# Performance work log

Hardware: AMD Instinct MI355X
Metric: run time of the kernel (lower is better)

The kernel has to match this reference:

```python
import jax, jax.numpy as jnp
import numpy as np
from jax import lax

EPS = 1e-5
DN = ('NCHW', 'OIHW', 'NCHW')


def _bn(x, gamma, beta, mean, var):
    # eval-mode BatchNorm2d over channel dim (axis=1)
    s = gamma / jnp.sqrt(var + EPS)
    return x * s[None, :, None, None] + (beta - mean * s)[None, :, None, None]


def setup_inputs() -> dict:
    key = jax.random.key(0)
    ks = jax.random.split(key, 12)
    B, Cin, C, H, W, NC = 128, 2048, 512, 14, 14, 200
    return {
        'feature': jax.random.normal(ks[0], (B, Cin, H, W), jnp.float32),
        'w_reduce': jax.random.normal(ks[1], (C, Cin, 1, 1), jnp.float32) * 0.02,
        'b_reduce': jax.random.normal(ks[2], (C,), jnp.float32) * 0.02,
        'bn1_gamma': jnp.ones((C,), jnp.float32),
        'bn1_beta': jnp.zeros((C,), jnp.float32),
        'bn1_mean': jax.random.normal(ks[3], (C,), jnp.float32) * 0.02,
        'bn1_var': jax.random.uniform(ks[4], (C,), jnp.float32),
        'w3': jax.random.normal(ks[5], (C, C, 3, 3), jnp.float32) * 0.02,
        'b3': jax.random.normal(ks[6], (C,), jnp.float32) * 0.02,
        'bn2_gamma': jnp.ones((C,), jnp.float32),
        'bn2_beta': jnp.zeros((C,), jnp.float32),
        'bn2_mean': jax.random.normal(ks[7], (C,), jnp.float32) * 0.02,
        'bn2_var': jax.random.uniform(ks[8], (C,), jnp.float32),
        'fc1_w': jax.random.normal(ks[9], (NC, C), jnp.float32) * 0.02,
        'fc1_b': jnp.zeros((NC,), jnp.float32),
        'fc2_w': jax.random.normal(ks[10], (NC, NC), jnp.float32) * 0.02,
        'fc2_b': jnp.zeros((NC,), jnp.float32),
    }


def reference(feature, w_reduce, b_reduce, bn1_gamma, bn1_beta, bn1_mean, bn1_var,
              w3, b3, bn2_gamma, bn2_beta, bn2_mean, bn2_var,
              fc1_w, fc1_b, fc2_w, fc2_b):
    B, _, H, W = feature.shape
    C = w_reduce.shape[0]  # 512
    # reduce: 1x1 conv + BN + ReLU
    f = lax.conv_general_dilated(feature, w_reduce, (1, 1), 'VALID', dimension_numbers=DN)
    f = f + b_reduce[None, :, None, None]
    f = jax.nn.relu(_bn(f, bn1_gamma, bn1_beta, bn1_mean, bn1_var))
    x = f.reshape(B, C, H * W)  # [B, 512, 196]
    # channel affinity + softmax(-xxt) over last dim (= the per-row loop)
    xxt = jnp.einsum('bcn,bdn->bcd', x, x)  # [B, 512, 512]
    a = jax.nn.softmax(-xxt, axis=2)
    y = jnp.einsum('bcd,bdn->bcn', a, x).reshape(B, C, H, W)
    # conv3: 3x3 conv + BN + ReLU + global avg pool
    z = lax.conv_general_dilated(y, w3, (1, 1), 'SAME', dimension_numbers=DN)
    z = z + b3[None, :, None, None]
    z = jax.nn.relu(_bn(z, bn2_gamma, bn2_beta, bn2_mean, bn2_var))
    z = jnp.mean(z, axis=(2, 3))  # [B, 512]
    # fc_channel: Linear -> ReLU -> Linear
    h = jax.nn.relu(z @ fc1_w.T + fc1_b)
    sf = h @ fc2_w.T + fc2_b
    return sf
```

## Files before the change

### kernel.cpp

```cpp
#include <hip/hip_runtime.h>

typedef __attribute__((ext_vector_type(8))) short bf16x8;
typedef __attribute__((ext_vector_type(4))) float f32x4;
typedef __attribute__((ext_vector_type(4))) short short4v;

__device__ __forceinline__ unsigned short f2bf(float x){
  unsigned u = __float_as_uint(x);
  return (unsigned short)((u + 0x7FFFu + ((u>>16)&1u)) >> 16);
}
__device__ __forceinline__ float bf2f(unsigned short b){
  return __uint_as_float(((unsigned)b)<<16);
}

typedef const __attribute__((address_space(1))) void* gas_t;
typedef __attribute__((address_space(3))) void* las_t;
__device__ __forceinline__ void gl16(const void* g, void* l){
  __builtin_amdgcn_global_load_lds((gas_t)g, (las_t)l, 16, 0, 0);
}

static constexpr size_t O_A    = 0;
static constexpr size_t O_FTLO = 29360128;
static constexpr size_t O_XHI  = 134217728;
static constexpr size_t O_XLO  = 167772160;
static constexpr size_t O_XT   = 201326592;
static constexpr size_t O_AMAT = 230686720;
static constexpr size_t O_WH   = 297795584;
static constexpr size_t O_WL   = 299892736;
static constexpr size_t O_W3B  = 301989888;
static constexpr size_t O_PAR  = 306708480;
static constexpr size_t O_FC1T = 306716672;
static constexpr size_t O_FC2T = 307126272;
static constexpr size_t O_ZBAR = 307286272;

__global__ void k_params(const float* br, const float* g1, const float* be1, const float* m1, const float* v1,
                         const float* b3, const float* g2, const float* be2, const float* m2, const float* v2,
                         float* par){
  int c = blockIdx.x*256 + threadIdx.x;
  if (c >= 512) return;
  float s1 = g1[c] * rsqrtf(v1[c] + 1e-5f);
  par[c] = s1;
  par[512+c] = (br[c]-m1[c])*s1 + be1[c];
  float s2 = g2[c] * rsqrtf(v2[c] + 1e-5f);
  par[1024+c] = s2;
  par[1536+c] = (b3[c]-m2[c])*s2 + be2[c];
}

__global__ void k_wrhl(const float* wr, unsigned short* wh, unsigned short* wl){
  int k = blockIdx.x*256 + threadIdx.x;
  int c = blockIdx.y;
  float v = wr[(size_t)c*2048 + k];
  unsigned short h = f2bf(v);
  wh[(size_t)c*2048 + k] = h;
  wl[(size_t)c*2048 + k] = f2bf(v - bf2f(h));
}

__global__ void k_w3c(const float* w3, unsigned short* w3c){
  int k = blockIdx.x*256 + threadIdx.x;
  int co = blockIdx.y;
  int ci0b = k/576; int r2 = k - ci0b*576;
  int tap = r2>>6;  int cio = r2&63;
  w3c[(((size_t)ci0b*9 + tap)*512 + co)*64 + cio] =
      f2bf(w3[((size_t)co*512 + ci0b*64 + cio)*9 + tap]);
}

__global__ void k_fc1t(const float* w, float* wt){
  int i = blockIdx.x*256 + threadIdx.x;
  int k = i/200, j = i - k*200;
  wt[i] = w[j*512 + k];
}
__global__ void k_fc2t(const float* w, float* wt){
  int i = blockIdx.x*256 + threadIdx.x;
  if (i >= 200*200) return;
  int k = i/200, j = i - k*200;
  wt[i] = w[j*200 + k];
}

__global__ __launch_bounds__(256) void k_featT(const float* __restrict__ feat,
        unsigned short* __restrict__ fhi, unsigned short* __restrict__ flo, int bbase){
  __shared__ float tile[64][33];
  int bloc = blockIdx.z;
  int b = bbase + bloc;
  int ci0 = blockIdx.y*64, p0 = blockIdx.x*32;
  int t = threadIdx.x;
  int j = t & 31, i0 = t >> 5;
  for (int rep=0; rep<8; ++rep){
    int i = rep*8 + i0;
    int p = p0 + j;
    tile[i][j] = (p<196) ? feat[((size_t)b*2048 + ci0 + i)*196 + p] : 0.f;
  }
  __syncthreads();
  int ii = t & 63, jj0 = t >> 6;
  for (int rep=0; rep<8; ++rep){
    int jj = rep*4 + jj0;
    float v = tile[ii][jj];
    unsigned short h = f2bf(v);
    size_t o = ((size_t)bloc*224 + p0 + jj)*2048 + ci0 + ii;
    fhi[o] = h;
    flo[o] = f2bf(v - bf2f(h));
  }
}

__global__ __launch_bounds__(256) void k_conv1(
    const unsigned short* __restrict__ fhi, const unsigned short* __restrict__ flo,
    const unsigned short* __restrict__ wh,  const unsigned short* __restrict__ wl,
    const float* __restrict__ par,
    unsigned short* __restrict__ xhi, unsigned short* __restrict__ xlo,
    unsigned short* __restrict__ xT, int bbase){
  __shared__ char lds[61440];
  char* AH = lds;
  char* ALo = lds + 16384;
  char* BH = lds + 32768;
  char* BLo = lds + 47104;
  int lin = blockIdx.x, per = gridDim.x>>3;
  int sz  = (lin&7)*per + (lin>>3);
  int bloc = sz>>3, sub = sz&7, mt = sub>>1, nt = sub&1;
  int b = bbase + bloc;
  int c0 = mt*128, n0 = nt*112;
  int t = threadIdx.x, lane = t&63, wid = t>>6;
  int fq = lane>>4, fr = lane&15;
  f32x4 acc[2][7] = {};
  const unsigned short* fbh = fhi + (size_t)bloc*224*2048;
  const unsigned short* fbl = flo + (size_t)bloc*224*2048;
  for (int it=0; it<32; ++it){
    int k0 = it*64;
    __syncthreads();
    #pragma unroll
    for (int r=0;r<4;++r){
      int L = r*256 + t;
      int row = L>>3, cs = ((L&7)^(row&7))*8;
      gl16(wh + (size_t)(c0+row)*2048 + k0 + cs, AH + L*16);
      gl16(wl + (size_t)(c0+row)*2048 + k0 + cs, ALo + L*16);
    }
    #pragma unroll
    for (int r=0;r<4;++r){
      int L = r*256 + t;
      if (L < 896){
        int row = L>>3, cs = ((L&7)^(row&7))*8;
        gl16(fbh + (size_t)(n0+row)*2048 + k0 + cs, BH + L*16);
        gl16(fbl + (size_t)(n0+row)*2048 + k0 + cs, BLo + L*16);
      }
    }
    __syncthreads();
    #pragma unroll
    for (int ks=0; ks<2; ++ks){
      int kb = ks*64 + fq*16;
      bf16x8 ah[2], al2[2];
      #pragma unroll
      for (int m=0;m<2;++m){
        int row = wid*32 + m*16 + fr;
        int off = row*128 + (kb ^ ((row&7)<<4));
        ah[m]  = *(const bf16x8*)(AH + off);
        al2[m] = *(const bf16x8*)(ALo + off);
      }
      #pragma unroll
      for (int n=0;n<7;++n){
        int row = n*16 + fr;
        int off = row*128 + (kb ^ ((row&7)<<4));
        bf16x8 bh  = *(const bf16x8*)(BH + off);
        bf16x8 bl2 = *(const bf16x8*)(BLo + off);
        #pragma unroll
        for (int m=0;m<2;++m){
          acc[m][n] = __builtin_amdgcn_mfma_f32_16x16x32_bf16(ah[m],  bh,  acc[m][n],0,0,0);
          acc[m][n] = __builtin_amdgcn_mfma_f32_16x16x32_bf16(ah[m],  bl2, acc[m][n],0,0,0);
          acc[m][n] = __builtin_amdgcn_mfma_f32_16x16x32_bf16(al2[m], bh,  acc[m][n],0,0,0);
        }
      }
    }
  }
  const float* s1 = par; const float* t1 = par+512;
  for (int m=0;m<2;++m){
    int cb = c0 + wid*32 + m*16 + fq*4;
    float sc[4], sh[4];
    for (int j=0;j<4;++j){ sc[j]=s1[cb+j]; sh[j]=t1[cb+j]; }
    for (int n=0;n<7;++n){
      int p = n0 + n*16 + fr;
      bool inb = p < 196;
      for (int j=0;j<4;++j){
        float v = inb ? fmaxf(acc[m][n][j]*sc[j]+sh[j], 0.f) : 0.f;
        unsigned short h  = f2bf(v);
        unsigned short lo = f2bf(v - bf2f(h));
        size_t ic = (size_t)b*512 + cb + j;
        xhi[ic*256 + p] = h;
        xlo[ic*256 + p] = lo;
        xT[((size_t)b*224 + p)*512 + cb + j] = h;
      }
    }
  }
}

__global__ __launch_bounds__(256) void k_xxt(const unsigned short* __restrict__ xhi,
        const unsigned short* __restrict__ xlo, float* __restrict__ xxt){
  __shared__ char lds[32768];
  char* Als = lds; char* Bls = lds + 16384;
  int lin = blockIdx.x;
  int sz  = (lin&7)*160 + (lin>>3);
  int b = sz/10, sub = sz - b*10;
  unsigned mtp = (3u<<18)|(2u<<16)|(2u<<14)|(1u<<12)|(1u<<10)|(1u<<8)|(0u<<6)|(0u<<4)|(0u<<2)|0u;
  unsigned ntp = (3u<<18)|(3u<<16)|(2u<<14)|(3u<<12)|(2u<<10)|(1u<<8)|(3u<<6)|(2u<<4)|(1u<<2)|0u;
  int mt = (mtp>>(2*sub))&3, nt = (ntp>>(2*sub))&3;
  int c0 = mt*128, d0 = nt*128;
  int t = threadIdx.x, lane = t&63, wid = t>>6, wm = wid&1, wn = wid>>1;
  int fq = lane>>4, fr = lane&15;
  f32x4 acc[4][4] = {};
  for (int it=0; it<12; ++it){
    int seg = it>>2, kk0 = (it&3)*64;
    const unsigned short* As = (seg<2) ? xhi : xlo;
    const unsigned short* Bs = (seg==1) ? xlo : xhi;
    __syncthreads();
    #pragma unroll
    for (int r=0;r<4;++r){
      int L = r*256 + t;
      int row = L>>3, cs = ((L&7)^(row&7))*8;
      gl16(As + ((size_t)b*512 + c0 + row)*256 + kk0 + cs, Als + L*16);
      gl16(Bs + ((size_t)b*512 + d0 + row)*256 + kk0 + cs, Bls + L*16);
    }
    __syncthreads();
    #pragma unroll
    for (int ks=0; ks<2; ++ks){
      int kb = ks*64 + fq*16;
      bf16x8 af[4];
      #pragma unroll
      for (int m=0;m<4;++m){
        int row = wm*64 + m*16 + fr;
        af[m] = *(const bf16x8*)(Als + row*128 + (kb ^ ((row&7)<<4)));
      }
      #pragma unroll
      for (int n=0;n<4;++n){
        int row = wn*64 + n*16 + fr;
        bf16x8 bff = *(const bf16x8*)(Bls + row*128 + (kb ^ ((row&7)<<4)));
        #pragma unroll
        for (int m=0;m<4;++m)
          acc[m][n] = __builtin_amdgcn_mfma_f32_16x16x32_bf16(af[m], bff, acc[m][n],0,0,0);
      }
    }
  }
  for (int m=0;m<4;++m){
    int cb = c0 + wm*64 + m*16 + fq*4;
    for (int n=0;n<4;++n){
      int d = d0 + wn*64 + n*16 + fr;
      *(float4*)(xxt + ((size_t)b*512 + d)*512 + cb) = *(float4*)&acc[m][n];
    }
  }
  if (mt != nt){
    for (int m=0;m<4;++m){
      int cb = c0 + wm*64 + m*16 + fq*4;
      for (int n=0;n<4;++n){
        int d = d0 + wn*64 + n*16 + fr;
        for (int jj=0;jj<4;++jj)
          xxt[((size_t)b*512 + cb + jj)*512 + d] = acc[m][n][jj];
      }
    }
  }
}

__global__ __launch_bounds__(256) void k_softmax(const float* __restrict__ xxt, unsigned short* __restrict__ amat){
  int row = blockIdx.x*4 + (threadIdx.x>>6);
  int lane = threadIdx.x & 63;
  const float* src = xxt + (size_t)row*512 + lane*8;
  float4 v0 = *(const float4*)src;
  float4 v1 = *(const float4*)(src+4);
  float mn = fminf(fminf(fminf(v0.x,v0.y),fminf(v0.z,v0.w)),
                   fminf(fminf(v1.x,v1.y),fminf(v1.z,v1.w)));
  for (int m=32; m; m>>=1) mn = fminf(mn, __shfl_xor(mn, m, 64));
  float e[8];
  e[0]=__expf(mn-v0.x); e[1]=__expf(mn-v0.y); e[2]=__expf(mn-v0.z); e[3]=__expf(mn-v0.w);
  e[4]=__expf(mn-v1.x); e[5]=__expf(mn-v1.y); e[6]=__expf(mn-v1.z); e[7]=__expf(mn-v1.w);
  float s = e[0]+e[1]+e[2]+e[3]+e[4]+e[5]+e[6]+e[7];
  for (int m=32; m; m>>=1) s += __shfl_xor(s, m, 64);
  float inv = 1.f/s;
  short4v p0, p1;
  for (int q=0;q<4;++q) p0[q] = (short)f2bf(e[q]*inv);
  for (int q=0;q<4;++q) p1[q] = (short)f2bf(e[4+q]*inv);
  unsigned short* dst = amat + (size_t)row*512 + lane*8;
  *(short4v*)dst = p0;
  *(short4v*)(dst+4) = p1;
}

__global__ __launch_bounds__(256) void k_pv(const unsigned short* __restrict__ amat,
        const unsigned short* __restrict__ xT, unsigned short* __restrict__ ypad){
  __shared__ char lds[30720];
  char* Als = lds; char* Bls = lds + 16384;
  int lin = blockIdx.x, per = gridDim.x>>3;
  int sz  = (lin&7)*per + (lin>>3);
  int b = sz>>3, sub = sz&7, mt = sub>>1, nt = sub&1;
  int c0 = mt*128, n0 = nt*112;
  int t = threadIdx.x, lane = t&63, wid = t>>6;
  int fq = lane>>4, fr = lane&15;
  f32x4 acc[2][7] = {};
  for (int it=0; it<8; ++it){
    int k0 = it*64;
    __syncthreads();
    #pragma unroll
    for (int r=0;r<4;++r){
      int L = r*256 + t;
      int row = L>>3, cs = ((L&7)^(row&7))*8;
      gl16(amat + ((size_t)b*512 + c0 + row)*512 + k0 + cs, Als + L*16);
    }
    #pragma unroll
    for (int r=0;r<4;++r){
      int L = r*256 + t;
      if (L < 896){
        int row = L>>3, cs = ((L&7)^(row&7))*8;
        gl16(xT + ((size_t)b*224 + n0 + row)*512 + k0 + cs, Bls + L*16);
      }
    }
    __syncthreads();
    #pragma unroll
    for (int ks=0; ks<2; ++ks){
      int kb = ks*64 + fq*16;
      bf16x8 af[2];
      #pragma unroll
      for (int m=0;m<2;++m){
        int row = wid*32 + m*16 + fr;
        af[m] = *(const bf16x8*)(Als + row*128 + (kb ^ ((row&7)<<4)));
      }
      #pragma unroll
      for (int n=0;n<7;++n){
        int row = n*16 + fr;
        bf16x8 bff = *(const bf16x8*)(Bls + row*128 + (kb ^ ((row&7)<<4)));
        #pragma unroll
        for (int m=0;m<2;++m)
          acc[m][n] = __builtin_amdgcn_mfma_f32_16x16x32_bf16(af[m], bff, acc[m][n],0,0,0);
      }
    }
  }
  for (int m=0;m<2;++m){
    int cb = c0 + wid*32 + m*16 + fq*4;
    int ci0b = cb>>6, cio = cb&63;
    for (int n=0;n<7;++n){
      int p = n0 + n*16 + fr;
      if (p < 196){
        int hh = p/14, wwp = p - hh*14;
        int prow = (hh+1)*16 + (wwp+1);
        short4v pk;
        for (int j=0;j<4;++j) pk[j] = (short)f2bf(acc[m][n][j]);
        *(short4v*)(ypad + (((size_t)b*8 + ci0b)*256 + prow)*64 + cio) = pk;
      }
    }
  }
}

__global__ __launch_bounds__(512, 4) void k_conv3(const unsigned short* __restrict__ ypad,
        const unsigned short* __restrict__ w3c, const float* __restrict__ par,
        float* __restrict__ zbar){
  __shared__ char lds[65536];
  char* WIN = lds;
  char* AB0 = lds + 32768;
  char* AB1 = lds + 49152;
  int bx = blockIdx.x;
  int xcd = bx&7, jj2 = bx>>3;
  int b = xcd*16 + (jj2>>2), cot = jj2&3;
  int c0 = cot*128;
  int t = threadIdx.x, lane = t&63, w = t>>6;
  int wm = w>>1, wn = w&1;
  int fq = lane>>4, fr = lane&15;
  int frB = (fr<14) ? fr : 13;
  bool pok = (fr<14);
  f32x4 acc[2][7] = {};
  for (int ci0=0; ci0<8; ++ci0){
    const unsigned short* wsrc = ypad + ((size_t)(b*8 + ci0)*256)*64;
    #pragma unroll
    for (int r=0;r<4;++r){
      int L = r*512 + t;
      int row = L>>3, cs = ((L&7)^(row&7))*8;
      gl16(wsrc + row*64 + cs, WIN + L*16);
    }
    {
      const unsigned short* asrc = w3c + ((size_t)(ci0*9 + 0)*512 + c0)*64;
      #pragma unroll
      for (int r=0;r<2;++r){
        int L = r*512 + t;
        int row = L>>3, cs = ((L&7)^(row&7))*8;
        gl16(asrc + row*64 + cs, AB0 + L*16);
      }
    }
    __syncthreads();
    for (int tap=0; tap<9; ++tap){
      char* Acur = (tap&1) ? AB1 : AB0;
      char* Anxt = (tap&1) ? AB0 : AB1;
      if (tap < 8){
        const unsigned short* asrc = w3c + ((size_t)(ci0*9 + tap+1)*512 + c0)*64;
        #pragma unroll
        for (int r=0;r<2;++r){
          int L = r*512 + t;
          int row = L>>3, cs = ((L&7)^(row&7))*8;
          gl16(asrc + row*64 + cs, Anxt + L*16);
        }
      }
      int kh = tap/3, kw = tap - kh*3;
      bf16x8 ah[2][2];
      #pragma unroll
      for (int ks=0;ks<2;++ks)
        #pragma unroll
        for (int m=0;m<2;++m){
          int row = wm*32 + m*16 + fr;
          ah[ks][m] = *(const bf16x8*)(Acur + row*128 + (((ks*4+fq)^(row&7))<<4));
        }
      int col = frB + kw;
      __builtin_amdgcn_s_setprio(1);
      #pragma unroll
      for (int n=0;n<7;++n){
        int prow = (wn*7 + n + kh)*16 + col;
        #pragma unroll
        for (int ks=0;ks<2;++ks){
          bf16x8 bf = *(const bf16x8*)(WIN + prow*128 + (((ks*4+fq)^(prow&7))<<4));
          acc[0][n] = __builtin_amdgcn_mfma_f32_16x16x32_bf16(ah[ks][0], bf, acc[0][n],0,0,0);
          acc[1][n] = __builtin_amdgcn_mfma_f32_16x16x32_bf16(ah[ks][1], bf, acc[1][n],0,0,0);
        }
      }
      __builtin_amdgcn_s_setprio(0);
      __syncthreads();
    }
  }
  const float* s2 = par+1024; const float* t2 = par+1536;
  float ps[2][4];
  #pragma unroll
  for (int m=0;m<2;++m){
    int cb = c0 + wm*32 + m*16 + fq*4;
    #pragma unroll
    for (int j=0;j<4;++j){
      float sc = s2[cb+j], sh = t2[cb+j];
      float s = 0.f;
      #pragma unroll
      for (int n=0;n<7;++n)
        s += fmaxf(acc[m][n][j]*sc + sh, 0.f);
      ps[m][j] = pok ? s : 0.f;
    }
  }
  #pragma unroll
  for (int off=1; off<16; off<<=1)
    #pragma unroll
    for (int m=0;m<2;++m)
      #pragma unroll
      for (int j=0;j<4;++j)
        ps[m][j] += __shfl_xor(ps[m][j], off, 64);
  float* part = (float*)lds;
  if (fr == 0){
    #pragma unroll
    for (int m=0;m<2;++m)
      #pragma unroll
      for (int j=0;j<4;++j)
        part[wn*128 + wm*32 + m*16 + fq*4 + j] = ps[m][j];
  }
  __syncthreads();
  if (t < 128)
    zbar[(size_t)b*512 + c0 + t] = part[t] + part[128 + t];
}

__global__ __launch_bounds__(256) void k_fc(const float* __restrict__ zbar,
        const float* __restrict__ fc1T, const float* __restrict__ fc1b,
        const float* __restrict__ fc2T, const float* __restrict__ fc2b,
        float* __restrict__ out){
  __shared__ float zb[512];
  __shared__ float hl[200];
  int b = blockIdx.x, t = threadIdx.x;
  zb[t]     = zbar[(size_t)b*512 + t]       * (1.f/196.f);
  zb[t+256] = zbar[(size_t)b*512 + t + 256] * (1.f/196.f);
  __syncthreads();
  if (t < 200){
    float acc = fc1b[t];
    for (int k=0;k<512;++k) acc += zb[k]*fc1T[k*200+t];
    hl[t] = fmaxf(acc, 0.f);
  }
  __syncthreads();
  if (t < 200){
    float acc = fc2b[t];
    for (int k=0;k<200;++k) acc += hl[k]*fc2T[k*200+t];
    out[(size_t)b*200 + t] = acc;
  }
}

extern "C" void kernel_launch(void* const* d_in, const int* in_sizes, int n_in,
                              void* d_out, int out_size, void* d_ws, size_t ws_size,
                              hipStream_t stream) {
  const float* feature  = (const float*)d_in[0];
  const float* w_reduce = (const float*)d_in[1];
  const float* b_reduce = (const float*)d_in[2];
  const float* g1  = (const float*)d_in[3];
  const float* be1 = (const float*)d_in[4];
  const float* m1  = (const float*)d_in[5];
  const float* v1  = (const float*)d_in[6];
  const float* w3  = (const float*)d_in[7];
  const float* b3  = (const float*)d_in[8];
  const float* g2  = (const float*)d_in[9];
  const float* be2 = (const float*)d_in[10];
  const float* m2  = (const float*)d_in[11];
  const float* v2  = (const float*)d_in[12];
  const float* fc1w = (const float*)d_in[13];
  const float* fc1b = (const float*)d_in[14];
  const float* fc2w = (const float*)d_in[15];
  const float* fc2b = (const float*)d_in[16];

  char* ws = (char*)d_ws;
  unsigned short* fhi  = (unsigned short*)(ws + O_A);
  unsigned short* flo  = (unsigned short*)(ws + O_FTLO);
  float*          xxt  = (float*)(ws + O_A);
  unsigned short* xhi  = (unsigned short*)(ws + O_XHI);
  unsigned short* xlo  = (unsigned short*)(ws + O_XLO);
  unsigned short* ypad = (unsigned short*)(ws + O_XLO);
  unsigned short* xT   = (unsigned short*)(ws + O_XT);
  unsigned short* amat = (unsigned short*)(ws + O_AMAT);
  unsigned short* wh   = (unsigned short*)(ws + O_WH);
  unsigned short* wl   = (unsigned short*)(ws + O_WL);
  unsigned short* w3c  = (unsigned short*)(ws + O_W3B);
  float* par  = (float*)(ws + O_PAR);
  float* fc1T = (float*)(ws + O_FC1T);
  float* fc2T = (float*)(ws + O_FC2T);
  float* zbar = (float*)(ws + O_ZBAR);

  hipMemsetAsync(xhi, 0, 33554432, stream);
  hipMemsetAsync(xlo, 0, 33554432, stream);

  k_params<<<2, 256, 0, stream>>>(b_reduce, g1, be1, m1, v1, b3, g2, be2, m2, v2, par);
  k_wrhl<<<dim3(8,512), 256, 0, stream>>>(w_reduce, wh, wl);
  k_w3c<<<dim3(18,512), 256, 0, stream>>>(w3, w3c);
  k_fc1t<<<400, 256, 0, stream>>>(fc1w, fc1T);
  k_fc2t<<<157, 256, 0, stream>>>(fc2w, fc2T);

  for (int ch = 0; ch < 4; ++ch){
    k_featT<<<dim3(7,32,32), 256, 0, stream>>>(feature, fhi, flo, ch*32);
    k_conv1<<<256, 256, 0, stream>>>(fhi, flo, wh, wl, par, xhi, xlo, xT, ch*32);
  }

  k_xxt<<<1280, 256, 0, stream>>>(xhi, xlo, xxt);
  k_softmax<<<16384, 256, 0, stream>>>(xxt, amat);

  hipMemsetAsync(ypad, 0, 33554432, stream);
  k_pv<<<1024, 256, 0, stream>>>(amat, xT, ypad);
  k_conv3<<<512, 512, 0, stream>>>(ypad, w3c, par, zbar);
  k_fc<<<128, 256, 0, stream>>>(zbar, fc1T, fc1b, fc2T, fc2b, (float*)d_out);
}
```

Before: 685.4 us.

## Flatten conv1 over batch-pixel GEMM with 128x128 tiles; replace full memsets with pad zeroing

The 1x1 reduce conv now runs as one GEMM over all 128*196 pixel columns without per-image padding to 224. It uses 128x128 tiles and runs the three hi/lo split products as consecutive K segments instead of three MFMAs per fragment, which removes the chunked 4-launch loop and the wasted padded columns. The full 32MB memsets are replaced by small kernels that zero only the pad regions of xhi/xlo and the border of ypad. The xT store is vectorised. The trade-offs are a larger workspace, since the whole fhi/flo for all batches is now materialised at once, and three times more K iterations per tile.

```diff
diff --git a/kernel.cpp b/kernel.cpp
--- a/kernel.cpp
+++ b/kernel.cpp
@@ -18,19 +18,19 @@
   __builtin_amdgcn_global_load_lds((gas_t)g, (las_t)l, 16, 0, 0);
 }
 
-static constexpr size_t O_A    = 0;
-static constexpr size_t O_FTLO = 29360128;
-static constexpr size_t O_XHI  = 134217728;
-static constexpr size_t O_XLO  = 167772160;
-static constexpr size_t O_XT   = 201326592;
-static constexpr size_t O_AMAT = 230686720;
-static constexpr size_t O_WH   = 297795584;
-static constexpr size_t O_WL   = 299892736;
-static constexpr size_t O_W3B  = 301989888;
-static constexpr size_t O_PAR  = 306708480;
-static constexpr size_t O_FC1T = 306716672;
-static constexpr size_t O_FC2T = 307126272;
-static constexpr size_t O_ZBAR = 307286272;
+static constexpr size_t O_FHI  = 0;
+static constexpr size_t O_FLO  = 102760448;
+static constexpr size_t O_XHI  = 205520896;
+static constexpr size_t O_XLO  = 239075328;
+static constexpr size_t O_XT   = 272629760;
+static constexpr size_t O_AMAT = 301989888;
+static constexpr size_t O_WH   = 369098752;
+static constexpr size_t O_WL   = 371195904;
+static constexpr size_t O_W3B  = 373293056;
+static constexpr size_t O_PAR  = 378011648;
+static constexpr size_t O_FC1T = 378019840;
+static constexpr size_t O_FC2T = 378429440;
+static constexpr size_t O_ZBAR = 378589440;
 
 __global__ void k_params(const float* br, const float* g1, const float* be1, const float* m1, const float* v1,
                          const float* b3, const float* g2, const float* be2, const float* m2, const float* v2,
@@ -75,11 +75,32 @@
   wt[i] = w[j*200 + k];
 }
 
+__global__ __launch_bounds__(256) void k_zeropad(unsigned short* xhi, unsigned short* xlo){
+  int rr = blockIdx.x*256 + threadIdx.x;
+  float4 z = {0.f,0.f,0.f,0.f};
+  float4* a = (float4*)(xhi + (size_t)rr*256 + 192);
+  float4* b = (float4*)(xlo + (size_t)rr*256 + 192);
+  #pragma unroll
+  for (int j=0;j<8;++j){ a[j] = z; b[j] = z; }
+}
+
+__global__ __launch_bounds__(256) void k_zeroyb(unsigned short* ypad){
+  int tile = blockIdx.x;
+  int r = threadIdx.x;
+  if (r >= 256) return;
+  int hi = r>>4, lo = r&15;
+  bool pad = (hi==0)||(hi==15)||(lo==0)||(lo==15);
+  if (!pad) return;
+  float4 z = {0.f,0.f,0.f,0.f};
+  float4* p = (float4*)(ypad + ((size_t)tile*256 + r)*64);
+  #pragma unroll
+  for (int j=0;j<8;++j) p[j] = z;
+}
+
 __global__ __launch_bounds__(256) void k_featT(const float* __restrict__ feat,
-        unsigned short* __restrict__ fhi, unsigned short* __restrict__ flo, int bbase){
+        unsigned short* __restrict__ fhi, unsigned short* __restrict__ flo){
   __shared__ float tile[64][33];
-  int bloc = blockIdx.z;
-  int b = bbase + bloc;
+  int b = blockIdx.z;
   int ci0 = blockIdx.y*64, p0 = blockIdx.x*32;
   int t = threadIdx.x;
   int j = t & 31, i0 = t >> 5;
@@ -92,11 +113,14 @@
   int ii = t & 63, jj0 = t >> 6;
   for (int rep=0; rep<8; ++rep){
     int jj = rep*4 + jj0;
-    float v = tile[ii][jj];
-    unsigned short h = f2bf(v);
-    size_t o = ((size_t)bloc*224 + p0 + jj)*2048 + ci0 + ii;
-    fhi[o] = h;
-    flo[o] = f2bf(v - bf2f(h));
+    int p = p0 + jj;
+    if (p < 196){
+      float v = tile[ii][jj];
+      unsigned short h = f2bf(v);
+      size_t o = ((size_t)b*196 + p)*2048 + ci0 + ii;
+      fhi[o] = h;
+      flo[o] = f2bf(v - bf2f(h));
+    }
   }
 }
 
@@ -105,85 +129,68 @@
     const unsigned short* __restrict__ wh,  const unsigned short* __restrict__ wl,
     const float* __restrict__ par,
     unsigned short* __restrict__ xhi, unsigned short* __restrict__ xlo,
-    unsigned short* __restrict__ xT, int bbase){
-  __shared__ char lds[61440];
-  char* AH = lds;
-  char* ALo = lds + 16384;
-  char* BH = lds + 32768;
-  char* BLo = lds + 47104;
-  int lin = blockIdx.x, per = gridDim.x>>3;
-  int sz  = (lin&7)*per + (lin>>3);
-  int bloc = sz>>3, sub = sz&7, mt = sub>>1, nt = sub&1;
-  int b = bbase + bloc;
-  int c0 = mt*128, n0 = nt*112;
-  int t = threadIdx.x, lane = t&63, wid = t>>6;
+    unsigned short* __restrict__ xT){
+  __shared__ char lds[32768];
+  char* Als = lds; char* Bls = lds + 16384;
+  int lin = blockIdx.x;
+  int sz  = (lin&7)*98 + (lin>>3);
+  int mt = sz&3;
+  int gt = sz>>2;
+  int c0 = mt*128;
+  size_t g0 = (size_t)gt*128;
+  int t = threadIdx.x, lane = t&63, wid = t>>6, wm = wid&1, wn = wid>>1;
   int fq = lane>>4, fr = lane&15;
-  f32x4 acc[2][7] = {};
-  const unsigned short* fbh = fhi + (size_t)bloc*224*2048;
-  const unsigned short* fbl = flo + (size_t)bloc*224*2048;
-  for (int it=0; it<32; ++it){
-    int k0 = it*64;
+  f32x4 acc[4][4] = {};
+  for (int it=0; it<96; ++it){
+    int seg = it>>5, kk0 = (it&31)*64;
+    const unsigned short* As = (seg<2) ? wh : wl;
+    const unsigned short* Bs = (seg==1) ? flo : fhi;
     __syncthreads();
     #pragma unroll
     for (int r=0;r<4;++r){
       int L = r*256 + t;
       int row = L>>3, cs = ((L&7)^(row&7))*8;
-      gl16(wh + (size_t)(c0+row)*2048 + k0 + cs, AH + L*16);
-      gl16(wl + (size_t)(c0+row)*2048 + k0 + cs, ALo + L*16);
-    }
-    #pragma unroll
-    for (int r=0;r<4;++r){
-      int L = r*256 + t;
-      if (L < 896){
-        int row = L>>3, cs = ((L&7)^(row&7))*8;
-        gl16(fbh + (size_t)(n0+row)*2048 + k0 + cs, BH + L*16);
-        gl16(fbl + (size_t)(n0+row)*2048 + k0 + cs, BLo + L*16);
-      }
+      gl16(As + (size_t)(c0+row)*2048 + kk0 + cs, Als + L*16);
+      gl16(Bs + (g0+row)*2048 + kk0 + cs, Bls + L*16);
     }
     __syncthreads();
     #pragma unroll
     for (int ks=0; ks<2; ++ks){
       int kb = ks*64 + fq*16;
-      bf16x8 ah[2], al2[2];
-      #pragma unroll
-      for (int m=0;m<2;++m){
-        int row = wid*32 + m*16 + fr;
-        int off = row*128 + (kb ^ ((row&7)<<4));
-        ah[m]  = *(const bf16x8*)(AH + off);
-        al2[m] = *(const bf16x8*)(ALo + off);
-      }
-      #pragma unroll
-      for (int n=0;n<7;++n){
-        int row = n*16 + fr;
-        int off = row*128 + (kb ^ ((row&7)<<4));
-        bf16x8 bh  = *(const bf16x8*)(BH + off);
-        bf16x8 bl2 = *(const bf16x8*)(BLo + off);
+      bf16x8 af[4];
+      #pragma unroll
+      for (int m=0;m<4;++m){
+        int row = wm*64 + m*16 + fr;
+        af[m] = *(const bf16x8*)(Als + row*128 + (kb ^ ((row&7)<<4)));
+      }
+      #pragma unroll
+      for (int n=0;n<4;++n){
+        int row = wn*64 + n*16 + fr;
+        bf16x8 bff = *(const bf16x8*)(Bls + row*128 + (kb ^ ((row&7)<<4)));
         #pragma unroll
-        for (int m=0;m<2;++m){
-          acc[m][n] = __builtin_amdgcn_mfma_f32_16x16x32_bf16(ah[m],  bh,  acc[m][n],0,0,0);
-          acc[m][n] = __builtin_amdgcn_mfma_f32_16x16x32_bf16(ah[m],  bl2, acc[m][n],0,0,0);
-          acc[m][n] = __builtin_amdgcn_mfma_f32_16x16x32_bf16(al2[m], bh,  acc[m][n],0,0,0);
-        }
+        for (int m=0;m<4;++m)
+          acc[m][n] = __builtin_amdgcn_mfma_f32_16x16x32_bf16(af[m], bff, acc[m][n],0,0,0);
       }
     }
   }
   const float* s1 = par; const float* t1 = par+512;
-  for (int m=0;m<2;++m){
-    int cb = c0 + wid*32 + m*16 + fq*4;
+  for (int m=0;m<4;++m){
+    int cb = c0 + wm*64 + m*16 + fq*4;
     float sc[4], sh[4];
     for (int j=0;j<4;++j){ sc[j]=s1[cb+j]; sh[j]=t1[cb+j]; }
-    for (int n=0;n<7;++n){
-      int p = n0 + n*16 + fr;
-      bool inb = p < 196;
+    for (int n=0;n<4;++n){
+      int gg = (int)g0 + wn*64 + n*16 + fr;
+      int b = gg/196, p = gg - b*196;
+      unsigned short hs[4];
       for (int j=0;j<4;++j){
-        float v = inb ? fmaxf(acc[m][n][j]*sc[j]+sh[j], 0.f) : 0.f;
-        unsigned short h  = f2bf(v);
-        unsigned short lo = f2bf(v - bf2f(h));
+        float v = fmaxf(acc[m][n][j]*sc[j]+sh[j], 0.f);
+        unsigned short h = f2bf(v);
+        hs[j] = h;
         size_t ic = (size_t)b*512 + cb + j;
         xhi[ic*256 + p] = h;
-        xlo[ic*256 + p] = lo;
-        xT[((size_t)b*224 + p)*512 + cb + j] = h;
-      }
+        xlo[ic*256 + p] = f2bf(v - bf2f(h));
+      }
+      *(short4v*)(xT + ((size_t)b*224 + p)*512 + cb) = *(short4v*)hs;
     }
   }
 }
@@ -492,9 +499,9 @@
   const float* fc2b = (const float*)d_in[16];
 
   char* ws = (char*)d_ws;
-  unsigned short* fhi  = (unsigned short*)(ws + O_A);
-  unsigned short* flo  = (unsigned short*)(ws + O_FTLO);
-  float*          xxt  = (float*)(ws + O_A);
+  unsigned short* fhi  = (unsigned short*)(ws + O_FHI);
+  unsigned short* flo  = (unsigned short*)(ws + O_FLO);
+  float*          xxt  = (float*)(ws + O_FHI);
   unsigned short* xhi  = (unsigned short*)(ws + O_XHI);
   unsigned short* xlo  = (unsigned short*)(ws + O_XLO);
   unsigned short* ypad = (unsigned short*)(ws + O_XLO);
@@ -508,24 +515,20 @@
   float* fc2T = (float*)(ws + O_FC2T);
   float* zbar = (float*)(ws + O_ZBAR);
 
-  hipMemsetAsync(xhi, 0, 33554432, stream);
-  hipMemsetAsync(xlo, 0, 33554432, stream);
-
   k_params<<<2, 256, 0, stream>>>(b_reduce, g1, be1, m1, v1, b3, g2, be2, m2, v2, par);
   k_wrhl<<<dim3(8,512), 256, 0, stream>>>(w_reduce, wh, wl);
   k_w3c<<<dim3(18,512), 256, 0, stream>>>(w3, w3c);
   k_fc1t<<<400, 256, 0, stream>>>(fc1w, fc1T);
   k_fc2t<<<157, 256, 0, stream>>>(fc2w, fc2T);
-
-  for (int ch = 0; ch < 4; ++ch){
-    k_featT<<<dim3(7,32,32), 256, 0, stream>>>(feature, fhi, flo, ch*32);
-    k_conv1<<<256, 256, 0, stream>>>(fhi, flo, wh, wl, par, xhi, xlo, xT, ch*32);
-  }
+  k_zeropad<<<256, 256, 0, stream>>>(xhi, xlo);
+
+  k_featT<<<dim3(7,32,128), 256, 0, stream>>>(feature, fhi, flo);
+  k_conv1<<<784, 256, 0, stream>>>(fhi, flo, wh, wl, par, xhi, xlo, xT);
 
   k_xxt<<<1280, 256, 0, stream>>>(xhi, xlo, xxt);
   k_softmax<<<16384, 256, 0, stream>>>(xxt, amat);
 
-  hipMemsetAsync(ypad, 0, 33554432, stream);
+  k_zeroyb<<<1024, 256, 0, stream>>>(ypad);
   k_pv<<<1024, 256, 0, stream>>>(amat, xT, ypad);
   k_conv3<<<512, 512, 0, stream>>>(ypad, w3c, par, zbar);
   k_fc<<<128, 256, 0, stream>>>(zbar, fc1T, fc1b, fc2T, fc2b, (float*)d_out);
```

Result: no change. 686.1 us (+0.1%).
